# Kernel optimization log

Measured on AMD Instinct MI355X. Metric: run time of the kernel, lower is better.

The kernel has to match this reference:

```python
import jax, jax.numpy as jnp
import numpy as np

B, S, DIM = 2, 2048, 1024
H = 16
HD = DIM // H  # 64
SCALE = HD ** -0.5


def setup_inputs() -> dict:
    key = jax.random.key(0)
    k1, k2, k3 = jax.random.split(key, 3)
    x = jax.random.normal(k1, (B, S, DIM), dtype=jnp.float32)
    # Linear weights scaled ~1/sqrt(fan_in) like torch default init
    Wqkv = jax.random.normal(k2, (DIM, 3 * DIM), dtype=jnp.float32) * (DIM ** -0.5)
    Wproj = jax.random.normal(k3, (DIM, DIM), dtype=jnp.float32) * (DIM ** -0.5)
    return {"x": x, "Wqkv": Wqkv, "Wproj": Wproj}


def reference(x, Wqkv, Wproj):
    Bsz, Slen, dim = x.shape
    qkv = x @ Wqkv  # (B, S, 3*dim)
    qkv = qkv.reshape(Bsz, Slen, 3, H, HD)
    q, k, v = qkv[:, :, 0], qkv[:, :, 1], qkv[:, :, 2]  # each (B, S, H, HD)
    # softmax attention (chunking in the original is memory-only; math identical)
    scores = jnp.einsum("bshd,bthd->bhst", q, k) * SCALE  # (B, H, S, S)
    attn = jax.nn.softmax(scores, axis=-1)
    out = jnp.einsum("bhst,bthd->bshd", attn, v)  # (B, S, H, HD)
    out = out.reshape(Bsz, Slen, dim)
    return out @ Wproj
```

## Files before the change

kernel.cpp:

```cpp
#include <hip/hip_runtime.h>
#include <stdint.h>

typedef unsigned short u16;
typedef __attribute__((ext_vector_type(8))) short bf16x8;
typedef __attribute__((ext_vector_type(4))) float f32x4;

#define BATCH 2
#define SEQ 2048
#define NH 16
#define HDIM 64
#define DMODEL 1024
#define MTOT (BATCH * SEQ)
#define QKV_N (3 * DMODEL)
#define ATT_SCALE 0.125f
#define L2E 1.44269504088896340736f
#define C2 (ATT_SCALE * L2E)

#define BAR() asm volatile("s_barrier" ::: "memory")
#define F3(a, b, c) fmaxf(fmaxf((a), (b)), (c))

__device__ __forceinline__ u16 f2b(float f) {
    uint32_t x = __builtin_bit_cast(uint32_t, f);
    uint32_t r = (x + 0x7fffu + ((x >> 16) & 1u)) >> 16;
    return (u16)r;
}

__device__ __forceinline__ uint32_t cvt_pk(float lo, float hi) {
    uint32_t r;
    asm("v_cvt_pk_bf16_f32 %0, %1, %2" : "=v"(r) : "v"(lo), "v"(hi));
    return r;
}

__device__ __forceinline__ void gl_lds16(const void* g, void* l) {
    __builtin_amdgcn_global_load_lds(
        (const __attribute__((address_space(1))) void*)g,
        (__attribute__((address_space(3))) void*)l, 16, 0, 0);
}

__global__ __launch_bounds__(256) void k_prep(const float* __restrict__ x,
                                              const float* __restrict__ Wq,
                                              const float* __restrict__ Wp,
                                              u16* __restrict__ xb,
                                              u16* __restrict__ WqT,
                                              u16* __restrict__ WpT) {
    const int bid = blockIdx.x, tid = threadIdx.x;
    if (bid < 2048) {
        const int i = bid * 256 + tid;
        const float4* p = (const float4*)x + (size_t)i * 2;
        float4 a = p[0], b = p[1];
        union { uint32_t w[4]; uint4 v; } u;
        u.w[0] = cvt_pk(a.x, a.y);
        u.w[1] = cvt_pk(a.z, a.w);
        u.w[2] = cvt_pk(b.x, b.y);
        u.w[3] = cvt_pk(b.z, b.w);
        *(uint4*)(xb + (size_t)i * 8) = u.v;
        return;
    }
    __shared__ float tile[64][65];
    const float* W;
    u16* WT;
    int cols, bx, by;
    if (bid < 2048 + 768) {
        const int j = bid - 2048;
        W = Wq; WT = WqT; cols = QKV_N; bx = j % 48; by = j / 48;
    } else {
        const int j = bid - 2816;
        W = Wp; WT = WpT; cols = DMODEL; bx = j % 16; by = j / 16;
    }
    const int rows = DMODEL;
    const int c0 = bx * 64, r0 = by * 64;
    const int tx = tid & 63, ty = tid >> 6;
#pragma unroll
    for (int i = 0; i < 16; ++i) {
        int r = i * 4 + ty;
        tile[r][tx] = W[(size_t)(r0 + r) * cols + c0 + tx];
    }
    __syncthreads();
#pragma unroll
    for (int i = 0; i < 16; ++i) {
        int c = i * 4 + ty;
        WT[(size_t)(c0 + c) * rows + r0 + tx] = f2b(tile[tx][c]);
    }
}

__global__ __launch_bounds__(512, 2) void k_gemm_qkv8(const u16* __restrict__ A,
                                                      const u16* __restrict__ BT,
                                                      u16* __restrict__ C,
                                                      u16* __restrict__ Vt) {
    extern __shared__ __align__(16) u16 lds[];
    const int tid = threadIdx.x, wid = tid >> 6, lane = tid & 63;
    const int r = lane & 15, g = lane >> 4;
    const int wr = wid >> 2, wc = wid & 3;
    const int m0 = blockIdx.y * 256, n0 = blockIdx.x * 256;
    const int K = DMODEL;

    auto STG = [&](int kt2, int rg) {
        const int isB = rg >> 1, half = rg & 1;
        const u16* src = isB ? BT : A;
        const int rowb = (isB ? n0 : m0) + half * 128 + wid * 16 + (lane >> 2);
        const u16* s = src + (size_t)rowb * K + kt2 * 64 + (lane & 3) * 8;
        const int dst = (kt2 & 1) * 32768 + isB * 16384 + half * 8192 +
                        wid * 1024 + lane * 8;
        gl_lds16(s, &lds[dst]);
        gl_lds16(s + 32, &lds[dst + 512]);
    };

    f32x4 acc[8][4] = {};
    bf16x8 a[4][2], b[4][2];
    const int aB = wr * 8192 + r * 32 + g * 8;
    const int bB = 16384 + (wc >> 1) * 8192 + (wc & 1) * 4096 + r * 32 + g * 8;

#pragma unroll
    for (int t2 = 0; t2 < 2; ++t2)
#pragma unroll
        for (int rg = 0; rg < 4; ++rg) STG(t2, rg);
    asm volatile("s_waitcnt vmcnt(0)" ::: "memory");
    __syncthreads();

    for (int kt = 0; kt < 16; ++kt) {
        const int sb = (kt & 1) * 32768;
#pragma unroll
        for (int mi = 0; mi < 4; ++mi)
#pragma unroll
            for (int kk = 0; kk < 2; ++kk)
                a[mi][kk] = *(const bf16x8*)&lds[sb + aB + (mi * 2 + kk) * 512];
#pragma unroll
        for (int ni = 0; ni < 2; ++ni)
#pragma unroll
            for (int kk = 0; kk < 2; ++kk)
                b[ni][kk] = *(const bf16x8*)&lds[sb + bB + (ni * 2 + kk) * 512];
        BAR();
        __builtin_amdgcn_s_setprio(1);
#pragma unroll
        for (int mi = 0; mi < 4; ++mi)
#pragma unroll
            for (int ni = 0; ni < 2; ++ni)
#pragma unroll
                for (int kk = 0; kk < 2; ++kk)
                    acc[mi][ni] = __builtin_amdgcn_mfma_f32_16x16x32_bf16(
                        b[ni][kk], a[mi][kk], acc[mi][ni], 0, 0, 0);
        __builtin_amdgcn_s_setprio(0);
        BAR();
#pragma unroll
        for (int ni = 2; ni < 4; ++ni)
#pragma unroll
            for (int kk = 0; kk < 2; ++kk)
                b[ni][kk] = *(const bf16x8*)&lds[sb + bB + (ni * 2 + kk) * 512];
        BAR();
        __builtin_amdgcn_s_setprio(1);
#pragma unroll
        for (int mi = 0; mi < 4; ++mi)
#pragma unroll
            for (int ni = 2; ni < 4; ++ni)
#pragma unroll
                for (int kk = 0; kk < 2; ++kk)
                    acc[mi][ni] = __builtin_amdgcn_mfma_f32_16x16x32_bf16(
                        b[ni][kk], a[mi][kk], acc[mi][ni], 0, 0, 0);
        __builtin_amdgcn_s_setprio(0);
        BAR();
#pragma unroll
        for (int mi = 0; mi < 4; ++mi)
#pragma unroll
            for (int kk = 0; kk < 2; ++kk)
                a[mi][kk] = *(const bf16x8*)&lds[sb + aB + ((4 + mi) * 2 + kk) * 512];
        if (kt < 14) { STG(kt + 2, 2); STG(kt + 2, 3); }
        BAR();
        __builtin_amdgcn_s_setprio(1);
#pragma unroll
        for (int mi = 0; mi < 4; ++mi)
#pragma unroll
            for (int ni = 2; ni < 4; ++ni)
#pragma unroll
                for (int kk = 0; kk < 2; ++kk)
                    acc[4 + mi][ni] = __builtin_amdgcn_mfma_f32_16x16x32_bf16(
                        b[ni][kk], a[mi][kk], acc[4 + mi][ni], 0, 0, 0);
        __builtin_amdgcn_s_setprio(0);
        BAR();
        if (kt < 14) { STG(kt + 2, 0); STG(kt + 2, 1); }
        BAR();
        __builtin_amdgcn_s_setprio(1);
#pragma unroll
        for (int mi = 0; mi < 4; ++mi)
#pragma unroll
            for (int ni = 0; ni < 2; ++ni)
#pragma unroll
                for (int kk = 0; kk < 2; ++kk)
                    acc[4 + mi][ni] = __builtin_amdgcn_mfma_f32_16x16x32_bf16(
                        b[ni][kk], a[mi][kk], acc[4 + mi][ni], 0, 0, 0);
        __builtin_amdgcn_s_setprio(0);
        if (kt < 14) {
            asm volatile("s_waitcnt vmcnt(8)" ::: "memory");
        } else if (kt == 14) {
            asm volatile("s_waitcnt vmcnt(0)" ::: "memory");
        }
        BAR();
    }

    if (n0 < 2 * DMODEL) {
#pragma unroll
        for (int mi = 0; mi < 8; ++mi)
#pragma unroll
            for (int ni = 0; ni < 4; ++ni) {
                const int row = m0 + wr * 128 + mi * 16 + r;
                const int col = n0 + wc * 64 + ni * 16 + g * 4;
                union { uint32_t w[2]; ushort4 v; } o;
                o.w[0] = cvt_pk(acc[mi][ni][0], acc[mi][ni][1]);
                o.w[1] = cvt_pk(acc[mi][ni][2], acc[mi][ni][3]);
                *(ushort4*)&C[(size_t)row * QKV_N + col] = o.v;
            }
    } else {
        const int h_ = ((n0 - 2 * DMODEL) >> 6) + wc;
#pragma unroll
        for (int mi = 0; mi < 8; ++mi)
#pragma unroll
            for (int ni = 0; ni < 4; ++ni) {
                const int row = m0 + wr * 128 + mi * 16 + r;
                const int b_ = row >> 11, s_ = row & (SEQ - 1);
                const int hd0 = ni * 16 + g * 4;
                union { uint32_t w[2]; u16 t[4]; } o;
                o.w[0] = cvt_pk(acc[mi][ni][0], acc[mi][ni][1]);
                o.w[1] = cvt_pk(acc[mi][ni][2], acc[mi][ni][3]);
                const size_t base =
                    ((size_t)(b_ * NH + h_) * HDIM + hd0) * SEQ + s_;
                Vt[base] = o.t[0];
                Vt[base + SEQ] = o.t[1];
                Vt[base + 2 * SEQ] = o.t[2];
                Vt[base + 3 * SEQ] = o.t[3];
            }
    }
}

__global__ __launch_bounds__(256) void k_gemm_proj(const u16* __restrict__ A,
                                                   const u16* __restrict__ BT,
                                                   float* __restrict__ C) {
    __shared__ __align__(16) u16 As[64 * 64];
    __shared__ __align__(16) u16 Bs[128 * 64];
    const int tid = threadIdx.x;
    const int wid = tid >> 6, lane = tid & 63;
    const int r = lane & 15, g = lane >> 4;
    const int m0 = blockIdx.y * 64, n0 = blockIdx.x * 128;
    const int srow = lane >> 3, scol = (lane & 7) * 8;
    const int K = DMODEL;
    f32x4 acc[4][2] = {};
    for (int k0 = 0; k0 < K; k0 += 64) {
#pragma unroll
        for (int i = 0; i < 2; ++i) {
            const int li = wid * 2 + i;
            gl_lds16(A + (size_t)(m0 + li * 8 + srow) * K + k0 + scol, &As[li * 512]);
        }
#pragma unroll
        for (int i = 0; i < 4; ++i) {
            const int li = wid * 4 + i;
            gl_lds16(BT + (size_t)(n0 + li * 8 + srow) * K + k0 + scol, &Bs[li * 512]);
        }
        __syncthreads();
#pragma unroll
        for (int kk = 0; kk < 2; ++kk) {
            bf16x8 af[4], bfr[2];
#pragma unroll
            for (int mi = 0; mi < 4; ++mi)
                af[mi] = *(const bf16x8*)&As[(mi * 16 + r) * 64 + kk * 32 + g * 8];
#pragma unroll
            for (int ni = 0; ni < 2; ++ni)
                bfr[ni] = *(const bf16x8*)&Bs[(wid * 32 + ni * 16 + r) * 64 + kk * 32 + g * 8];
#pragma unroll
            for (int mi = 0; mi < 4; ++mi)
#pragma unroll
                for (int ni = 0; ni < 2; ++ni)
                    acc[mi][ni] = __builtin_amdgcn_mfma_f32_16x16x32_bf16(
                        bfr[ni], af[mi], acc[mi][ni], 0, 0, 0);
        }
        __syncthreads();
    }
#pragma unroll
    for (int mi = 0; mi < 4; ++mi)
#pragma unroll
        for (int ni = 0; ni < 2; ++ni) {
            const int row = m0 + mi * 16 + r;
            const int col = n0 + wid * 32 + ni * 16 + g * 4;
            float4 vv;
            vv.x = acc[mi][ni][0]; vv.y = acc[mi][ni][1];
            vv.z = acc[mi][ni][2]; vv.w = acc[mi][ni][3];
            *(float4*)&C[(size_t)row * DMODEL + col] = vv;
        }
}

__global__ __launch_bounds__(256) void k_attn(const u16* __restrict__ qkv,
                                              const u16* __restrict__ Vt,
                                              u16* __restrict__ O) {
    __shared__ __align__(16) u16 Ks[2][4096];
    __shared__ __align__(16) u16 Vs[2][4096];
    const int bh = blockIdx.y;
    const int b = bh >> 4, h = bh & 15;
    const int q0 = blockIdx.x * 64;
    const int tid = threadIdx.x, wid = tid >> 6, lane = tid & 63;
    const int r = lane & 15, g = lane >> 4;

    const size_t qbase = (size_t)(b * SEQ + q0 + wid * 16 + r) * QKV_N + h * HDIM;
    const bf16x8 qf0 = *(const bf16x8*)&qkv[qbase + g * 8];
    const bf16x8 qf1 = *(const bf16x8*)&qkv[qbase + 32 + g * 8];

    const short one_b = (short)0x3F80;
    const bf16x8 ones = {one_b, one_b, one_b, one_b, one_b, one_b, one_b, one_b};

    float mL = -1e30f;
    f32x4 oacc[4] = {};
    f32x4 lacc = {};
    const int kc0 = wid * 2;

    const u16* kp[2];
    const u16* vp[2];
    int kdst[2], vdst[2];
#pragma unroll
    for (int i = 0; i < 2; ++i) {
        const int kc = kc0 + i;
        const int ksrow = (kc >> 2) * 32 + g * 8 + (kc & 1) * 4 + ((lane >> 2) & 3);
        const int kscol = ((kc >> 1) & 1) * 32 + (lane & 3) * 8;
        kp[i] = qkv + (size_t)(b * SEQ + ksrow) * QKV_N + DMODEL + h * HDIM + kscol;
        const int vhd = (kc & 3) * 16 + r;
        const int vsc = (kc >> 2) * 32 + g * 8;
        vp[i] = Vt + ((size_t)bh * HDIM + vhd) * SEQ + vsc;
        kdst[i] = kc * 512;
        vdst[i] = kc * 512;
    }

#define STAGE_K(BUF)                                                 \
    {                                                                \
        _Pragma("unroll") for (int i = 0; i < 2; ++i) {              \
            gl_lds16(kp[i], &Ks[BUF][kdst[i]]);                      \
            kp[i] += 64 * QKV_N;                                     \
        }                                                            \
    }
#define STAGE_V(BUF)                                                 \
    {                                                                \
        _Pragma("unroll") for (int i = 0; i < 2; ++i) {              \
            gl_lds16(vp[i], &Vs[BUF][vdst[i]]);                      \
            vp[i] += 64;                                             \
        }                                                            \
    }

    STAGE_K(0); STAGE_V(0);
    STAGE_K(1); STAGE_V(1);
    asm volatile("s_waitcnt vmcnt(0)");
    __syncthreads();

    for (int t = 0; t < SEQ / 64; ++t) {
        const int cur = t & 1;

        f32x4 sacc[4] = {};
        __builtin_amdgcn_s_setprio(1);
#pragma unroll
        for (int nf = 0; nf < 4; ++nf) {
            const int kbase = (nf & 1) * 2048 + (nf >> 1) * 512 +
                              (r >> 2) * 128 + (r & 3) * 32 + g * 8;
            bf16x8 kf0 = *(const bf16x8*)&Ks[cur][kbase];
            bf16x8 kf1 = *(const bf16x8*)&Ks[cur][kbase + 1024];
            sacc[nf] = __builtin_amdgcn_mfma_f32_16x16x32_bf16(kf0, qf0, sacc[nf], 0, 0, 0);
            sacc[nf] = __builtin_amdgcn_mfma_f32_16x16x32_bf16(kf1, qf1, sacc[nf], 0, 0, 0);
        }
        __builtin_amdgcn_s_setprio(0);
        BAR();
        if (t < SEQ / 64 - 2) STAGE_K(cur);

        float mt = F3(sacc[0][0], sacc[0][1], sacc[0][2]);
        mt = F3(mt, sacc[0][3], sacc[1][0]);
        mt = F3(mt, sacc[1][1], sacc[1][2]);
        mt = F3(mt, sacc[1][3], sacc[2][0]);
        mt = F3(mt, sacc[2][1], sacc[2][2]);
        mt = F3(mt, sacc[2][3], sacc[3][0]);
        mt = F3(mt, sacc[3][1], sacc[3][2]);
        mt = fmaxf(mt, sacc[3][3]);
        const float pm = mt * C2;
        if (!__all(pm <= mL + 8.f)) {
            float rm = pm;
            rm = fmaxf(rm, __shfl_xor(rm, 16, 64));
            rm = fmaxf(rm, __shfl_xor(rm, 32, 64));
            const float mNew = fmaxf(mL, rm);
            const float al = exp2f(mL - mNew);
            mL = mNew;
#pragma unroll
            for (int ht = 0; ht < 4; ++ht)
#pragma unroll
                for (int e = 0; e < 4; ++e) oacc[ht][e] *= al;
#pragma unroll
            for (int e = 0; e < 4; ++e) lacc[e] *= al;
        }
        float p[4][4];
#pragma unroll
        for (int nf = 0; nf < 4; ++nf)
#pragma unroll
            for (int e = 0; e < 4; ++e)
                p[nf][e] = exp2f(sacc[nf][e] * C2 - mL);

        union { uint32_t w[4]; bf16x8 v; } upf0, upf1;
        upf0.w[0] = cvt_pk(p[0][0], p[0][1]);
        upf0.w[1] = cvt_pk(p[0][2], p[0][3]);
        upf0.w[2] = cvt_pk(p[2][0], p[2][1]);
        upf0.w[3] = cvt_pk(p[2][2], p[2][3]);
        upf1.w[0] = cvt_pk(p[1][0], p[1][1]);
        upf1.w[1] = cvt_pk(p[1][2], p[1][3]);
        upf1.w[2] = cvt_pk(p[3][0], p[3][1]);
        upf1.w[3] = cvt_pk(p[3][2], p[3][3]);

        __builtin_amdgcn_s_setprio(1);
#pragma unroll
        for (int ht = 0; ht < 4; ++ht) {
            bf16x8 vf0 = *(const bf16x8*)&Vs[cur][ht * 512 + g * 128 + r * 8];
            bf16x8 vf1 = *(const bf16x8*)&Vs[cur][(4 + ht) * 512 + g * 128 + r * 8];
            oacc[ht] = __builtin_amdgcn_mfma_f32_16x16x32_bf16(vf0, upf0.v, oacc[ht], 0, 0, 0);
            oacc[ht] = __builtin_amdgcn_mfma_f32_16x16x32_bf16(vf1, upf1.v, oacc[ht], 0, 0, 0);
        }
        lacc = __builtin_amdgcn_mfma_f32_16x16x32_bf16(ones, upf0.v, lacc, 0, 0, 0);
        lacc = __builtin_amdgcn_mfma_f32_16x16x32_bf16(ones, upf1.v, lacc, 0, 0, 0);
        __builtin_amdgcn_s_setprio(0);
        BAR();
        if (t < SEQ / 64 - 2) {
            STAGE_V(cur);
            asm volatile("s_waitcnt vmcnt(4)");
        } else if (t == SEQ / 64 - 2) {
            asm volatile("s_waitcnt vmcnt(0)");
        }
        if (t < SEQ / 64 - 1) BAR();
    }
#undef STAGE_K
#undef STAGE_V

    const float inv = 1.0f / lacc[0];
    const size_t obase = (size_t)(b * SEQ + q0 + wid * 16 + r) * DMODEL + h * HDIM;
#pragma unroll
    for (int ht = 0; ht < 4; ++ht) {
        union { uint32_t w[2]; ushort4 v; } o;
        o.w[0] = cvt_pk(oacc[ht][0] * inv, oacc[ht][1] * inv);
        o.w[1] = cvt_pk(oacc[ht][2] * inv, oacc[ht][3] * inv);
        *(ushort4*)&O[obase + ht * 16 + g * 4] = o.v;
    }
}

extern "C" void kernel_launch(void* const* d_in, const int* in_sizes, int n_in,
                              void* d_out, int out_size, void* d_ws, size_t ws_size,
                              hipStream_t stream) {
    const float* x = (const float*)d_in[0];
    const float* Wqkv = (const float*)d_in[1];
    const float* Wproj = (const float*)d_in[2];
    float* out = (float*)d_out;

    u16* xb = (u16*)d_ws;
    u16* WqkvT = xb + (size_t)MTOT * DMODEL;
    u16* WprojT = WqkvT + (size_t)QKV_N * DMODEL;
    u16* qkv = WprojT + (size_t)DMODEL * DMODEL;
    u16* Vt = qkv + (size_t)MTOT * QKV_N;
    u16* Ob = Vt + (size_t)BATCH * NH * HDIM * SEQ;

    hipFuncSetAttribute(reinterpret_cast<const void*>(k_gemm_qkv8),
                        hipFuncAttributeMaxDynamicSharedMemorySize, 131072);

    k_prep<<<dim3(3072), 256, 0, stream>>>(x, Wqkv, Wproj, xb, WqkvT, WprojT);
    k_gemm_qkv8<<<dim3(QKV_N / 256, MTOT / 256), 512, 131072, stream>>>(
        xb, WqkvT, qkv, Vt);
    k_attn<<<dim3(SEQ / 64, BATCH * NH), 256, 0, stream>>>(qkv, Vt, Ob);
    k_gemm_proj<<<dim3(DMODEL / 128, MTOT / 64), 256, 0, stream>>>(Ob, WprojT, out);
}
```

Baseline: 214.6 us.

## Software-pipeline QK^T one tile ahead with triple-buffered K in attention

Adds a third K shared-memory buffer and computes the QK^T scores for the next key tile while the current tile's softmax and PV MFMAs run. The MFMA work for the scores can then overlap the exp/max VALU work inside a wavefront, and one barrier per iteration is removed. The cost is extra registers for the second score accumulator and 8KB more LDS, which may reduce occupancy. The wait-count bookkeeping also becomes more intricate.

```diff
diff --git a/kernel.cpp b/kernel.cpp
--- a/kernel.cpp
+++ b/kernel.cpp
@@ -288,13 +288,14 @@
 __global__ __launch_bounds__(256) void k_attn(const u16* __restrict__ qkv,
                                               const u16* __restrict__ Vt,
                                               u16* __restrict__ O) {
-    __shared__ __align__(16) u16 Ks[2][4096];
+    __shared__ __align__(16) u16 Ks[3][4096];
     __shared__ __align__(16) u16 Vs[2][4096];
     const int bh = blockIdx.y;
     const int b = bh >> 4, h = bh & 15;
     const int q0 = blockIdx.x * 64;
     const int tid = threadIdx.x, wid = tid >> 6, lane = tid & 63;
     const int r = lane & 15, g = lane >> 4;
+    const int NT = SEQ / 64;
 
     const size_t qbase = (size_t)(b * SEQ + q0 + wid * 16 + r) * QKV_N + h * HDIM;
     const bf16x8 qf0 = *(const bf16x8*)&qkv[qbase + g * 8];
@@ -324,52 +325,67 @@
         vdst[i] = kc * 512;
     }
 
-#define STAGE_K(BUF)                                                 \
+#define STAGE_K(SLOT)                                                \
     {                                                                \
         _Pragma("unroll") for (int i = 0; i < 2; ++i) {              \
-            gl_lds16(kp[i], &Ks[BUF][kdst[i]]);                      \
+            gl_lds16(kp[i], &Ks[SLOT][kdst[i]]);                     \
             kp[i] += 64 * QKV_N;                                     \
         }                                                            \
     }
-#define STAGE_V(BUF)                                                 \
+#define STAGE_V(SLOT)                                                \
     {                                                                \
         _Pragma("unroll") for (int i = 0; i < 2; ++i) {              \
-            gl_lds16(vp[i], &Vs[BUF][vdst[i]]);                      \
+            gl_lds16(vp[i], &Vs[SLOT][vdst[i]]);                     \
             vp[i] += 64;                                             \
         }                                                            \
     }
+#define QKT(DST, SLOT)                                               \
+    {                                                                \
+        _Pragma("unroll") for (int nf = 0; nf < 4; ++nf) {           \
+            const int kbase = (nf & 1) * 2048 + (nf >> 1) * 512 +    \
+                              (r >> 2) * 128 + (r & 3) * 32 + g * 8; \
+            bf16x8 kf0 = *(const bf16x8*)&Ks[SLOT][kbase];           \
+            bf16x8 kf1 = *(const bf16x8*)&Ks[SLOT][kbase + 1024];    \
+            DST[nf] = __builtin_amdgcn_mfma_f32_16x16x32_bf16(       \
+                kf0, qf0, DST[nf], 0, 0, 0);                         \
+            DST[nf] = __builtin_amdgcn_mfma_f32_16x16x32_bf16(       \
+                kf1, qf1, DST[nf], 0, 0, 0);                         \
+        }                                                            \
+    }
 
     STAGE_K(0); STAGE_V(0);
     STAGE_K(1); STAGE_V(1);
+    STAGE_K(2);
     asm volatile("s_waitcnt vmcnt(0)");
     __syncthreads();
 
-    for (int t = 0; t < SEQ / 64; ++t) {
-        const int cur = t & 1;
-
-        f32x4 sacc[4] = {};
-        __builtin_amdgcn_s_setprio(1);
-#pragma unroll
-        for (int nf = 0; nf < 4; ++nf) {
-            const int kbase = (nf & 1) * 2048 + (nf >> 1) * 512 +
-                              (r >> 2) * 128 + (r & 3) * 32 + g * 8;
-            bf16x8 kf0 = *(const bf16x8*)&Ks[cur][kbase];
-            bf16x8 kf1 = *(const bf16x8*)&Ks[cur][kbase + 1024];
-            sacc[nf] = __builtin_amdgcn_mfma_f32_16x16x32_bf16(kf0, qf0, sacc[nf], 0, 0, 0);
-            sacc[nf] = __builtin_amdgcn_mfma_f32_16x16x32_bf16(kf1, qf1, sacc[nf], 0, 0, 0);
-        }
-        __builtin_amdgcn_s_setprio(0);
-        BAR();
-        if (t < SEQ / 64 - 2) STAGE_K(cur);
-
-        float mt = F3(sacc[0][0], sacc[0][1], sacc[0][2]);
-        mt = F3(mt, sacc[0][3], sacc[1][0]);
-        mt = F3(mt, sacc[1][1], sacc[1][2]);
-        mt = F3(mt, sacc[1][3], sacc[2][0]);
-        mt = F3(mt, sacc[2][1], sacc[2][2]);
-        mt = F3(mt, sacc[2][3], sacc[3][0]);
-        mt = F3(mt, sacc[3][1], sacc[3][2]);
-        mt = fmaxf(mt, sacc[3][3]);
+    f32x4 sA[4] = {};
+    __builtin_amdgcn_s_setprio(1);
+    QKT(sA, 0);
+    __builtin_amdgcn_s_setprio(0);
+    BAR();
+
+    int kw = 0, kr = 1;
+    for (int t = 0; t < NT; ++t) {
+        const int vcur = t & 1;
+
+        if (t + 3 < NT) STAGE_K(kw);
+
+        f32x4 sB[4] = {};
+        if (t + 1 < NT) {
+            __builtin_amdgcn_s_setprio(1);
+            QKT(sB, kr);
+            __builtin_amdgcn_s_setprio(0);
+        }
+
+        float mt = F3(sA[0][0], sA[0][1], sA[0][2]);
+        mt = F3(mt, sA[0][3], sA[1][0]);
+        mt = F3(mt, sA[1][1], sA[1][2]);
+        mt = F3(mt, sA[1][3], sA[2][0]);
+        mt = F3(mt, sA[2][1], sA[2][2]);
+        mt = F3(mt, sA[2][3], sA[3][0]);
+        mt = F3(mt, sA[3][1], sA[3][2]);
+        mt = fmaxf(mt, sA[3][3]);
         const float pm = mt * C2;
         if (!__all(pm <= mL + 8.f)) {
             float rm = pm;
@@ -390,7 +406,7 @@
         for (int nf = 0; nf < 4; ++nf)
 #pragma unroll
             for (int e = 0; e < 4; ++e)
-                p[nf][e] = exp2f(sacc[nf][e] * C2 - mL);
+                p[nf][e] = exp2f(sA[nf][e] * C2 - mL);
 
         union { uint32_t w[4]; bf16x8 v; } upf0, upf1;
         upf0.w[0] = cvt_pk(p[0][0], p[0][1]);
@@ -405,25 +421,36 @@
         __builtin_amdgcn_s_setprio(1);
 #pragma unroll
         for (int ht = 0; ht < 4; ++ht) {
-            bf16x8 vf0 = *(const bf16x8*)&Vs[cur][ht * 512 + g * 128 + r * 8];
-            bf16x8 vf1 = *(const bf16x8*)&Vs[cur][(4 + ht) * 512 + g * 128 + r * 8];
+            bf16x8 vf0 = *(const bf16x8*)&Vs[vcur][ht * 512 + g * 128 + r * 8];
+            bf16x8 vf1 = *(const bf16x8*)&Vs[vcur][(4 + ht) * 512 + g * 128 + r * 8];
             oacc[ht] = __builtin_amdgcn_mfma_f32_16x16x32_bf16(vf0, upf0.v, oacc[ht], 0, 0, 0);
             oacc[ht] = __builtin_amdgcn_mfma_f32_16x16x32_bf16(vf1, upf1.v, oacc[ht], 0, 0, 0);
         }
         lacc = __builtin_amdgcn_mfma_f32_16x16x32_bf16(ones, upf0.v, lacc, 0, 0, 0);
         lacc = __builtin_amdgcn_mfma_f32_16x16x32_bf16(ones, upf1.v, lacc, 0, 0, 0);
         __builtin_amdgcn_s_setprio(0);
-        BAR();
-        if (t < SEQ / 64 - 2) {
-            STAGE_V(cur);
-            asm volatile("s_waitcnt vmcnt(4)");
-        } else if (t == SEQ / 64 - 2) {
-            asm volatile("s_waitcnt vmcnt(0)");
-        }
-        if (t < SEQ / 64 - 1) BAR();
+
+        if (t + 1 < NT) {
+            BAR();
+            if (t + 2 < NT) STAGE_V(vcur);
+            if (t <= NT - 4) {
+                asm volatile("s_waitcnt vmcnt(4)");
+            } else if (t == NT - 3) {
+                asm volatile("s_waitcnt vmcnt(2)");
+            } else {
+                asm volatile("s_waitcnt vmcnt(0)");
+            }
+            BAR();
+        }
+
+#pragma unroll
+        for (int nf = 0; nf < 4; ++nf) sA[nf] = sB[nf];
+        kw = (kw == 2) ? 0 : kw + 1;
+        kr = (kr == 2) ? 0 : kr + 1;
     }
 #undef STAGE_K
 #undef STAGE_V
+#undef QKT
 
     const float inv = 1.0f / lacc[0];
     const size_t obase = (size_t)(b * SEQ + q0 + wid * 16 + r) * DMODEL + h * HDIM;
```

Result: no change. 215.0 us (+0.2%).
